# Kernel optimization log

Hardware: AMD Instinct MI355X
Metric: run time of the kernel (lower is better)

## Reference

```python
import jax, jax.numpy as jnp
import numpy as np

EMBED_DIM = 1024
NUM_HEADS = 16
HEAD_DIM = EMBED_DIM // NUM_HEADS


def setup_inputs() -> dict:
    key = jax.random.key(0)
    ks = jax.random.split(key, 5)
    B, S, D = 2, 2048, EMBED_DIM
    scale = 1.0 / np.sqrt(D)
    x = jax.random.normal(ks[0], (B, S, D), dtype=jnp.float32)
    qkv_w = jax.random.uniform(ks[1], (3 * D, D), dtype=jnp.float32, minval=-scale, maxval=scale)
    qkv_b = jax.random.uniform(ks[2], (3 * D,), dtype=jnp.float32, minval=-scale, maxval=scale)
    out_w = jax.random.uniform(ks[3], (D, D), dtype=jnp.float32, minval=-scale, maxval=scale)
    out_b = jax.random.uniform(ks[4], (D,), dtype=jnp.float32, minval=-scale, maxval=scale)
    return {"x": x, "qkv_w": qkv_w, "qkv_b": qkv_b, "out_w": out_w, "out_b": out_b}


def reference(x, qkv_w, qkv_b, out_w, out_b):
    B, S, D = x.shape
    H, hd = NUM_HEADS, HEAD_DIM
    # QKV projection (torch Linear: y = x @ W^T + b)
    qkv = jnp.einsum('bsd,ed->bse', x, qkv_w) + qkv_b          # [B,S,3D]
    qkv = qkv.reshape(B, S, 3, H, hd)
    q, k, v = (jnp.moveaxis(qkv[:, :, i], 2, 1) for i in range(3))  # each [B,H,S,hd]
    scores = jnp.einsum('bhqd,bhkd->bhqk', q, k) / np.sqrt(hd)  # [B,H,S,S]
    probs = jax.nn.softmax(scores, axis=-1)
    attn = jnp.einsum('bhqk,bhkd->bhqd', probs, v)              # [B,H,S,hd]
    attn = jnp.moveaxis(attn, 1, 2).reshape(B, S, D)
    return jnp.einsum('bsd,ed->bse', attn, out_w) + out_b
```

## Files before the change

### kernel.cpp

```cpp
#include <hip/hip_runtime.h>
#include <stdint.h>

typedef __bf16 bf16;
typedef __attribute__((ext_vector_type(4))) __bf16 bf16x4;
typedef __attribute__((ext_vector_type(8))) __bf16 bf16x8;
typedef __attribute__((ext_vector_type(4))) float f32x4;

#define LOG2E_OVER_8 0.18033688011112042f

__device__ __forceinline__ void gl_lds16(const bf16* g, bf16* l) {
  __builtin_amdgcn_global_load_lds(
      (const __attribute__((address_space(1))) void*)g,
      (__attribute__((address_space(3))) void*)l, 16, 0, 0);
}
#define WAIT_VM0_BARRIER() asm volatile("s_waitcnt vmcnt(0)\n\ts_barrier" ::: "memory")

__global__ __launch_bounds__(256) void cvt_kernel(const float* __restrict__ s,
                                                  bf16* __restrict__ d, int n) {
  int i = (blockIdx.x * 256 + threadIdx.x) * 8;
  if (i >= n) return;
  float4 a = *(const float4*)(s + i);
  float4 b = *(const float4*)(s + i + 4);
  bf16x8 o;
  o[0] = (bf16)a.x; o[1] = (bf16)a.y; o[2] = (bf16)a.z; o[3] = (bf16)a.w;
  o[4] = (bf16)b.x; o[5] = (bf16)b.y; o[6] = (bf16)b.z; o[7] = (bf16)b.w;
  *(bf16x8*)(d + i) = o;
}

template <int EPI>
__global__ __launch_bounds__(256, 2) void gemm_bt(
    const bf16* __restrict__ A, const bf16* __restrict__ Bw,
    const float* __restrict__ bias,
    bf16* __restrict__ qo, bf16* __restrict__ ko, bf16* __restrict__ vTo,
    float* __restrict__ outF) {
  constexpr int MT = EPI ? 64 : 128;
  constexpr int MI = MT / 32;
  constexpr int ASZ = MT * 32;
  constexpr int BSZ = 128 * 32;
  constexpr int RS = 136;
  constexpr int SME = EPI ? (2 * ASZ + 2 * BSZ) : (128 * RS);
  __shared__ __attribute__((aligned(16))) bf16 smem[SME];

  const int t = threadIdx.x;
  const int L = t & 63;
  const int li = L & 15;
  const int qd = L >> 4;
  const int w = t >> 6;
  const int wm = (w >> 1) * (MT / 2);
  const int wn = (w & 1) * 64;
  const int bm0 = blockIdx.y * MT;
  const int bn0 = blockIdx.x * 128;
  const int r_st = t >> 2;
  const int c_st = (t & 3) * 8;

  const bf16* Ab = A + (size_t)bm0 * 1024;
  const bf16* Bb = Bw + (size_t)bn0 * 1024;

  auto issue = [&](int k0, int bi) {
    bf16* As_ = smem + bi * ASZ;
    bf16* Bs_ = smem + 2 * ASZ + bi * BSZ;
    gl_lds16(Ab + (size_t)r_st * 1024 + k0 + c_st, As_ + t * 8);
    if constexpr (MT == 128)
      gl_lds16(Ab + (size_t)(r_st + 64) * 1024 + k0 + c_st, As_ + (t + 256) * 8);
    gl_lds16(Bb + (size_t)r_st * 1024 + k0 + c_st, Bs_ + t * 8);
    gl_lds16(Bb + (size_t)(r_st + 64) * 1024 + k0 + c_st, Bs_ + (t + 256) * 8);
  };

  f32x4 acc[MI][4] = {};
  issue(0, 0);
  for (int it = 0; it < 32; ++it) {
    WAIT_VM0_BARRIER();
    if (it < 31) issue((it + 1) * 32, (it + 1) & 1);
    const bf16* Ac = smem + (it & 1) * ASZ;
    const bf16* Bc = smem + 2 * ASZ + (it & 1) * BSZ;
    bf16x8 af[MI], bfr[4];
#pragma unroll
    for (int mi = 0; mi < MI; ++mi)
      af[mi] = *(const bf16x8*)(Ac + (wm + mi * 16 + li) * 32 + qd * 8);
#pragma unroll
    for (int ni = 0; ni < 4; ++ni)
      bfr[ni] = *(const bf16x8*)(Bc + (wn + ni * 16 + li) * 32 + qd * 8);
#pragma unroll
    for (int mi = 0; mi < MI; ++mi)
#pragma unroll
      for (int ni = 0; ni < 4; ++ni)
        acc[mi][ni] = __builtin_amdgcn_mfma_f32_16x16x32_bf16(af[mi], bfr[ni],
                                                              acc[mi][ni], 0, 0, 0);
  }

  if constexpr (EPI == 0) {
    const int which = bn0 >> 10;
    __syncthreads();
    bf16* Ct = smem;
    if (which == 2) {
#pragma unroll
      for (int mi = 0; mi < MI; ++mi) {
        const int m_l = wm + mi * 16 + qd * 4;
#pragma unroll
        for (int ni = 0; ni < 4; ++ni) {
          const int n_l = wn + ni * 16 + li;
          const float bi = bias[bn0 + n_l];
          bf16x4 pk;
#pragma unroll
          for (int r = 0; r < 4; ++r) pk[r] = (bf16)(acc[mi][ni][r] + bi);
          *(bf16x4*)(Ct + n_l * RS + m_l) = pk;
        }
      }
    } else {
      const float sc = (which == 0) ? LOG2E_OVER_8 : 1.0f;
#pragma unroll
      for (int mi = 0; mi < MI; ++mi) {
        const int m_l = wm + mi * 16 + qd * 4;
#pragma unroll
        for (int ni = 0; ni < 4; ++ni) {
          const int n_l = wn + ni * 16 + li;
          const float bi = bias[bn0 + n_l];
#pragma unroll
          for (int r = 0; r < 4; ++r)
            Ct[(m_l + r) * RS + n_l] = (bf16)((acc[mi][ni][r] + bi) * sc);
        }
      }
    }
    __syncthreads();
    const int jr = t >> 4;
    const int jc = t & 15;
#pragma unroll
    for (int pass = 0; pass < 8; ++pass) {
      const int row = pass * 16 + jr;
      bf16x8 vv = *(const bf16x8*)(Ct + row * RS + jc * 8);
      if (which == 2) {
        const int n_g = bn0 + row;
        const int hh = (n_g >> 6) & 15, dd = n_g & 63;
        const int bb = bm0 >> 11;
        const int s_b = (bm0 & 2047) + jc * 8;
        *(bf16x8*)(vTo + ((size_t)(bb * 16 + hh) * 64 + dd) * 2048 + s_b) = vv;
      } else {
        const int m_g = bm0 + row;
        const int bb = m_g >> 11, ss = m_g & 2047;
        const int n_g = bn0 + jc * 8;
        const int hh = (n_g >> 6) & 15, dd = n_g & 63;
        bf16* dst = (which == 0 ? qo : ko);
        *(bf16x8*)(dst + ((size_t)(bb * 16 + hh) * 2048 + ss) * 64 + dd) = vv;
      }
    }
  } else {
#pragma unroll
    for (int mi = 0; mi < MI; ++mi) {
      const int m_g = bm0 + wm + mi * 16 + qd * 4;
#pragma unroll
      for (int ni = 0; ni < 4; ++ni) {
        const int n_g = bn0 + wn + ni * 16 + li;
        const float bi = bias[n_g];
#pragma unroll
        for (int r = 0; r < 4; ++r)
          outF[(size_t)(m_g + r) * 1024 + n_g] = acc[mi][ni][r] + bi;
      }
    }
  }
}

__global__ __launch_bounds__(256, 2) void attn_fwd(
    const bf16* __restrict__ Q, const bf16* __restrict__ K,
    const bf16* __restrict__ VT, bf16* __restrict__ AO) {
  __shared__ __attribute__((aligned(16))) bf16 Ks[2 * 4096];
  __shared__ __attribute__((aligned(16))) bf16 Vs[2 * 4096];
  __shared__ __attribute__((aligned(16))) bf16 Ps[4 * 2048];
  const int t = threadIdx.x;
  const int L = t & 63;
  const int li = L & 15;
  const int qd = L >> 4;
  const int w = t >> 6;

  const int lid = blockIdx.x + (blockIdx.y << 4) + (blockIdx.z << 8);
  const int slot = lid >> 3;
  const int bh_ = ((lid & 7) << 2) + (slot >> 4);
  const int qb = slot & 15;
  const int b = bh_ >> 4, h = bh_ & 15;
  const size_t bh = (size_t)(b * 16 + h);

  const bf16* Qp = Q + bh * 2048 * 64;
  const bf16* Kp = K + bh * 2048 * 64;
  const bf16* Vp = VT + bh * 64 * 2048;
  const int q0 = qb * 128 + w * 32;

  bf16x8 qf[2][2];
#pragma unroll
  for (int mi = 0; mi < 2; ++mi)
#pragma unroll
    for (int kk = 0; kk < 2; ++kk)
      qf[mi][kk] = *(const bf16x8*)(Qp + (size_t)(q0 + mi * 16 + li) * 64 + kk * 32 + qd * 8);

  f32x4 O[2][4] = {};
  float lsum[2] = {0.f, 0.f};
  bf16* Pw = Ps + w * 2048;
  const int r_st = t >> 2;
  const int c_st = (t & 3) * 8;
  const f32x4 zf = {0.f, 0.f, 0.f, 0.f};

  auto issue = [&](int kt, int bi) {
    const bf16* Kt = Kp + (size_t)kt * 4096;
    const bf16* Vt = Vp + kt * 64;
    bf16* Kd = Ks + bi * 4096;
    bf16* Vd = Vs + bi * 4096;
    gl_lds16(Kt + (size_t)r_st * 64 + c_st, Kd + t * 8);
    gl_lds16(Kt + (size_t)r_st * 64 + 32 + c_st, Kd + (t + 256) * 8);
    gl_lds16(Vt + (size_t)r_st * 2048 + c_st, Vd + t * 8);
    gl_lds16(Vt + (size_t)r_st * 2048 + 32 + c_st, Vd + (t + 256) * 8);
  };

  issue(0, 0);
  for (int kt = 0; kt < 32; ++kt) {
    WAIT_VM0_BARRIER();
    if (kt < 31) issue(kt + 1, (kt + 1) & 1);
    const bf16* Kc = Ks + (kt & 1) * 4096;
    const bf16* Vc = Vs + (kt & 1) * 4096;

    f32x4 sc[4][2];
#pragma unroll
    for (int ki = 0; ki < 4; ++ki) {
      bf16x8 kf0 = *(const bf16x8*)(Kc + (ki * 16 + li) * 32 + qd * 8);
      bf16x8 kf1 = *(const bf16x8*)(Kc + 2048 + (ki * 16 + li) * 32 + qd * 8);
#pragma unroll
      for (int mi = 0; mi < 2; ++mi) {
        f32x4 tmp = __builtin_amdgcn_mfma_f32_16x16x32_bf16(kf0, qf[mi][0], zf, 0, 0, 0);
        sc[ki][mi] = __builtin_amdgcn_mfma_f32_16x16x32_bf16(kf1, qf[mi][1], tmp, 0, 0, 0);
      }
    }

#pragma unroll
    for (int ki = 0; ki < 4; ++ki)
#pragma unroll
      for (int mi = 0; mi < 2; ++mi) {
        bf16x4 pk;
        float s0 = 0.f;
#pragma unroll
        for (int r = 0; r < 4; ++r) {
          float p = exp2f(fminf(sc[ki][mi][r], 80.f));
          s0 += p;
          pk[r] = (bf16)p;
        }
        lsum[mi] += s0;
        const int row = mi * 16 + li;
        const int chunk = 2 * ki + (qd >> 1);
        *(bf16x4*)(Pw + row * 64 + ((chunk ^ (row & 7)) << 3) + ((qd & 1) << 2)) = pk;
      }

    asm volatile("s_waitcnt lgkmcnt(0)" ::: "memory");

#pragma unroll
    for (int ks = 0; ks < 2; ++ks) {
      const int r0 = li, r1 = 16 + li;
      bf16x8 pf0 = *(const bf16x8*)(Pw + r0 * 64 + (((ks * 4 + qd) ^ (r0 & 7)) << 3));
      bf16x8 pf1 = *(const bf16x8*)(Pw + r1 * 64 + (((ks * 4 + qd) ^ (r1 & 7)) << 3));
#pragma unroll
      for (int nd = 0; nd < 4; ++nd) {
        bf16x8 vf = *(const bf16x8*)(Vc + ks * 2048 + (nd * 16 + li) * 32 + qd * 8);
        O[0][nd] = __builtin_amdgcn_mfma_f32_16x16x32_bf16(pf0, vf, O[0][nd], 0, 0, 0);
        O[1][nd] = __builtin_amdgcn_mfma_f32_16x16x32_bf16(pf1, vf, O[1][nd], 0, 0, 0);
      }
    }
  }

  float ls[2];
#pragma unroll
  for (int mi = 0; mi < 2; ++mi) {
    float v = lsum[mi];
    v += __shfl_xor(v, 16);
    v += __shfl_xor(v, 32);
    ls[mi] = v;
  }

#pragma unroll
  for (int mi = 0; mi < 2; ++mi) {
#pragma unroll
    for (int r = 0; r < 4; ++r) {
      const float inv = 1.f / __shfl(ls[mi], qd * 4 + r);
      const int row = q0 + mi * 16 + qd * 4 + r;
      const size_t base = ((size_t)b * 2048 + row) * 1024 + h * 64;
#pragma unroll
      for (int nd = 0; nd < 4; ++nd)
        AO[base + nd * 16 + li] = (bf16)(O[mi][nd][r] * inv);
    }
  }
}

extern "C" void kernel_launch(void* const* d_in, const int* in_sizes, int n_in,
                              void* d_out, int out_size, void* d_ws, size_t ws_size,
                              hipStream_t stream) {
  const float* x = (const float*)d_in[0];
  const float* qkvw = (const float*)d_in[1];
  const float* qkvb = (const float*)d_in[2];
  const float* outw = (const float*)d_in[3];
  const float* outb = (const float*)d_in[4];
  float* out = (float*)d_out;

  bf16* xb = (bf16*)d_ws;
  bf16* wq = xb + (size_t)4096 * 1024;
  bf16* wo = wq + (size_t)3072 * 1024;
  bf16* q = wo + (size_t)1024 * 1024;
  bf16* kk = q + (size_t)2 * 16 * 2048 * 64;
  bf16* vT = kk + (size_t)2 * 16 * 2048 * 64;
  bf16* attn = xb;

  cvt_kernel<<<2048, 256, 0, stream>>>(x, xb, 4096 * 1024);
  cvt_kernel<<<1536, 256, 0, stream>>>(qkvw, wq, 3072 * 1024);
  cvt_kernel<<<512, 256, 0, stream>>>(outw, wo, 1024 * 1024);

  gemm_bt<0><<<dim3(24, 32), 256, 0, stream>>>(xb, wq, qkvb, q, kk, vT, nullptr);
  attn_fwd<<<dim3(16, 16, 2), 256, 0, stream>>>(q, kk, vT, attn);
  gemm_bt<1><<<dim3(8, 64), 256, 0, stream>>>(attn, wo, outb, nullptr, nullptr, nullptr, out);
}
```

Before: 210.6 us.

## Switch attention to 32x32x16 MFMA with register-resident P via lane shuffles

Rewrites the attention inner loop to use 32x32x16 bf16 MFMAs, computing S transposed so each lane holds a key column for its query row. The probabilities are repacked into the PV operand layout with cross-half-wave shuffles, so the P round-trip through LDS goes away, and K/V tiles are now stored with an XOR swizzle. It also drops the clamp before exp2 and raises the launch bound to 3 waves per SIMD for both kernels, which may cause register spills.

```diff
diff --git a/kernel.cpp b/kernel.cpp
--- a/kernel.cpp
+++ b/kernel.cpp
@@ -2,9 +2,11 @@
 #include <stdint.h>
 
 typedef __bf16 bf16;
+typedef __attribute__((ext_vector_type(2))) __bf16 bf16x2;
 typedef __attribute__((ext_vector_type(4))) __bf16 bf16x4;
 typedef __attribute__((ext_vector_type(8))) __bf16 bf16x8;
 typedef __attribute__((ext_vector_type(4))) float f32x4;
+typedef __attribute__((ext_vector_type(16))) float f32x16;
 
 #define LOG2E_OVER_8 0.18033688011112042f
 
@@ -14,6 +16,12 @@
       (__attribute__((address_space(3))) void*)l, 16, 0, 0);
 }
 #define WAIT_VM0_BARRIER() asm volatile("s_waitcnt vmcnt(0)\n\ts_barrier" ::: "memory")
+
+__device__ __forceinline__ uint32_t pack2(float a, float b) {
+  union { bf16x2 v; uint32_t u; } z;
+  z.v[0] = (bf16)a; z.v[1] = (bf16)b;
+  return z.u;
+}
 
 __global__ __launch_bounds__(256) void cvt_kernel(const float* __restrict__ s,
                                                   bf16* __restrict__ d, int n) {
@@ -28,7 +36,7 @@
 }
 
 template <int EPI>
-__global__ __launch_bounds__(256, 2) void gemm_bt(
+__global__ __launch_bounds__(256, 3) void gemm_bt(
     const bf16* __restrict__ A, const bf16* __restrict__ Bw,
     const float* __restrict__ bias,
     bf16* __restrict__ qo, bf16* __restrict__ ko, bf16* __restrict__ vTo,
@@ -159,16 +167,15 @@
   }
 }
 
-__global__ __launch_bounds__(256, 2) void attn_fwd(
+__global__ __launch_bounds__(256, 3) void attn_fwd(
     const bf16* __restrict__ Q, const bf16* __restrict__ K,
     const bf16* __restrict__ VT, bf16* __restrict__ AO) {
   __shared__ __attribute__((aligned(16))) bf16 Ks[2 * 4096];
   __shared__ __attribute__((aligned(16))) bf16 Vs[2 * 4096];
-  __shared__ __attribute__((aligned(16))) bf16 Ps[4 * 2048];
   const int t = threadIdx.x;
   const int L = t & 63;
-  const int li = L & 15;
-  const int qd = L >> 4;
+  const int m31 = L & 31;
+  const int hi = L >> 5;
   const int w = t >> 6;
 
   const int lid = blockIdx.x + (blockIdx.y << 4) + (blockIdx.z << 8);
@@ -183,31 +190,28 @@
   const bf16* Vp = VT + bh * 64 * 2048;
   const int q0 = qb * 128 + w * 32;
 
-  bf16x8 qf[2][2];
-#pragma unroll
-  for (int mi = 0; mi < 2; ++mi)
-#pragma unroll
-    for (int kk = 0; kk < 2; ++kk)
-      qf[mi][kk] = *(const bf16x8*)(Qp + (size_t)(q0 + mi * 16 + li) * 64 + kk * 32 + qd * 8);
-
-  f32x4 O[2][4] = {};
-  float lsum[2] = {0.f, 0.f};
-  bf16* Pw = Ps + w * 2048;
-  const int r_st = t >> 2;
-  const int c_st = (t & 3) * 8;
-  const f32x4 zf = {0.f, 0.f, 0.f, 0.f};
-
+  bf16x8 qf[4];
+#pragma unroll
+  for (int s = 0; s < 4; ++s)
+    qf[s] = *(const bf16x8*)(Qp + (size_t)(q0 + m31) * 64 + s * 16 + hi * 8);
+
+  f32x16 acc[2] = {};
+  float lsum = 0.f;
+
+  const int srow = t >> 3;
+  const int scc = (t & 7) ^ (srow & 7);
   auto issue = [&](int kt, int bi) {
     const bf16* Kt = Kp + (size_t)kt * 4096;
     const bf16* Vt = Vp + kt * 64;
     bf16* Kd = Ks + bi * 4096;
     bf16* Vd = Vs + bi * 4096;
-    gl_lds16(Kt + (size_t)r_st * 64 + c_st, Kd + t * 8);
-    gl_lds16(Kt + (size_t)r_st * 64 + 32 + c_st, Kd + (t + 256) * 8);
-    gl_lds16(Vt + (size_t)r_st * 2048 + c_st, Vd + t * 8);
-    gl_lds16(Vt + (size_t)r_st * 2048 + 32 + c_st, Vd + (t + 256) * 8);
+    gl_lds16(Kt + srow * 64 + scc * 8, Kd + t * 8);
+    gl_lds16(Kt + (srow + 32) * 64 + scc * 8, Kd + (t + 256) * 8);
+    gl_lds16(Vt + (size_t)srow * 2048 + scc * 8, Vd + t * 8);
+    gl_lds16(Vt + (size_t)(srow + 32) * 2048 + scc * 8, Vd + (t + 256) * 8);
   };
 
+  const int rlow = m31 & 7;
   issue(0, 0);
   for (int kt = 0; kt < 32; ++kt) {
     WAIT_VM0_BARRIER();
@@ -215,72 +219,77 @@
     const bf16* Kc = Ks + (kt & 1) * 4096;
     const bf16* Vc = Vs + (kt & 1) * 4096;
 
-    f32x4 sc[4][2];
-#pragma unroll
-    for (int ki = 0; ki < 4; ++ki) {
-      bf16x8 kf0 = *(const bf16x8*)(Kc + (ki * 16 + li) * 32 + qd * 8);
-      bf16x8 kf1 = *(const bf16x8*)(Kc + 2048 + (ki * 16 + li) * 32 + qd * 8);
-#pragma unroll
-      for (int mi = 0; mi < 2; ++mi) {
-        f32x4 tmp = __builtin_amdgcn_mfma_f32_16x16x32_bf16(kf0, qf[mi][0], zf, 0, 0, 0);
-        sc[ki][mi] = __builtin_amdgcn_mfma_f32_16x16x32_bf16(kf1, qf[mi][1], tmp, 0, 0, 0);
-      }
-    }
-
-#pragma unroll
-    for (int ki = 0; ki < 4; ++ki)
-#pragma unroll
-      for (int mi = 0; mi < 2; ++mi) {
-        bf16x4 pk;
-        float s0 = 0.f;
-#pragma unroll
-        for (int r = 0; r < 4; ++r) {
-          float p = exp2f(fminf(sc[ki][mi][r], 80.f));
-          s0 += p;
-          pk[r] = (bf16)p;
+    f32x16 st[2];
+#pragma unroll
+    for (int kt2 = 0; kt2 < 2; ++kt2) {
+      f32x16 z = {};
+#pragma unroll
+      for (int s = 0; s < 4; ++s) {
+        bf16x8 kf = *(const bf16x8*)(
+            Kc + ((kt2 * 32 + m31) * 8 + ((2 * s + hi) ^ rlow)) * 8);
+        z = __builtin_amdgcn_mfma_f32_32x32x16_bf16(kf, qf[s], z, 0, 0, 0);
+      }
+      st[kt2] = z;
+    }
+
+    uint32_t pk[2][8];
+#pragma unroll
+    for (int kt2 = 0; kt2 < 2; ++kt2)
+#pragma unroll
+      for (int j = 0; j < 8; ++j) {
+        float a = exp2f(st[kt2][2 * j]);
+        float c = exp2f(st[kt2][2 * j + 1]);
+        lsum += a + c;
+        pk[kt2][j] = pack2(a, c);
+      }
+
+    uint32_t sw[2][8];
+#pragma unroll
+    for (int kt2 = 0; kt2 < 2; ++kt2)
+#pragma unroll
+      for (int j = 0; j < 8; ++j)
+        sw[kt2][j] = (uint32_t)__shfl_xor((int)pk[kt2][j], 32);
+
+    union FU { uint32_t u[4]; bf16x8 v; };
+    FU af[2][2];
+#pragma unroll
+    for (int kt2 = 0; kt2 < 2; ++kt2) {
+      if (hi == 0) {
+        af[kt2][0].u[0] = pk[kt2][0]; af[kt2][0].u[1] = pk[kt2][1];
+        af[kt2][0].u[2] = sw[kt2][0]; af[kt2][0].u[3] = sw[kt2][1];
+        af[kt2][1].u[0] = pk[kt2][4]; af[kt2][1].u[1] = pk[kt2][5];
+        af[kt2][1].u[2] = sw[kt2][4]; af[kt2][1].u[3] = sw[kt2][5];
+      } else {
+        af[kt2][0].u[0] = sw[kt2][2]; af[kt2][0].u[1] = sw[kt2][3];
+        af[kt2][0].u[2] = pk[kt2][2]; af[kt2][0].u[3] = pk[kt2][3];
+        af[kt2][1].u[0] = sw[kt2][6]; af[kt2][1].u[1] = sw[kt2][7];
+        af[kt2][1].u[2] = pk[kt2][6]; af[kt2][1].u[3] = pk[kt2][7];
+      }
+    }
+
+#pragma unroll
+    for (int dt = 0; dt < 2; ++dt)
+#pragma unroll
+      for (int kt2 = 0; kt2 < 2; ++kt2)
+#pragma unroll
+        for (int u = 0; u < 2; ++u) {
+          bf16x8 vf = *(const bf16x8*)(
+              Vc + ((dt * 32 + m31) * 8 + ((kt2 * 4 + u * 2 + hi) ^ rlow)) * 8);
+          acc[dt] = __builtin_amdgcn_mfma_f32_32x32x16_bf16(af[kt2][u].v, vf,
+                                                            acc[dt], 0, 0, 0);
         }
-        lsum[mi] += s0;
-        const int row = mi * 16 + li;
-        const int chunk = 2 * ki + (qd >> 1);
-        *(bf16x4*)(Pw + row * 64 + ((chunk ^ (row & 7)) << 3) + ((qd & 1) << 2)) = pk;
-      }
-
-    asm volatile("s_waitcnt lgkmcnt(0)" ::: "memory");
-
-#pragma unroll
-    for (int ks = 0; ks < 2; ++ks) {
-      const int r0 = li, r1 = 16 + li;
-      bf16x8 pf0 = *(const bf16x8*)(Pw + r0 * 64 + (((ks * 4 + qd) ^ (r0 & 7)) << 3));
-      bf16x8 pf1 = *(const bf16x8*)(Pw + r1 * 64 + (((ks * 4 + qd) ^ (r1 & 7)) << 3));
-#pragma unroll
-      for (int nd = 0; nd < 4; ++nd) {
-        bf16x8 vf = *(const bf16x8*)(Vc + ks * 2048 + (nd * 16 + li) * 32 + qd * 8);
-        O[0][nd] = __builtin_amdgcn_mfma_f32_16x16x32_bf16(pf0, vf, O[0][nd], 0, 0, 0);
-        O[1][nd] = __builtin_amdgcn_mfma_f32_16x16x32_bf16(pf1, vf, O[1][nd], 0, 0, 0);
-      }
-    }
   }
 
-  float ls[2];
-#pragma unroll
-  for (int mi = 0; mi < 2; ++mi) {
-    float v = lsum[mi];
-    v += __shfl_xor(v, 16);
-    v += __shfl_xor(v, 32);
-    ls[mi] = v;
-  }
-
-#pragma unroll
-  for (int mi = 0; mi < 2; ++mi) {
-#pragma unroll
-    for (int r = 0; r < 4; ++r) {
-      const float inv = 1.f / __shfl(ls[mi], qd * 4 + r);
-      const int row = q0 + mi * 16 + qd * 4 + r;
-      const size_t base = ((size_t)b * 2048 + row) * 1024 + h * 64;
-#pragma unroll
-      for (int nd = 0; nd < 4; ++nd)
-        AO[base + nd * 16 + li] = (bf16)(O[mi][nd][r] * inv);
-    }
+  lsum += __shfl_xor(lsum, 32);
+  const float inv = 1.f / lsum;
+
+#pragma unroll
+  for (int r = 0; r < 16; ++r) {
+    const int qrow = (r & 3) + 8 * (r >> 2) + 4 * hi;
+    const float invq = __shfl(inv, qrow);
+    const size_t base = ((size_t)b * 2048 + q0 + qrow) * 1024 + h * 64 + m31;
+    AO[base] = (bf16)(acc[0][r] * invq);
+    AO[base + 32] = (bf16)(acc[1][r] * invq);
   }
 }
 
```

Measured after the change: 203.3 us. -3.5%, faster.
